# Kernel optimization log

Hardware: AMD Instinct MI355X
Metric: run time of the kernel (lower is better)

The kernel has to match this reference:

```python
import jax, jax.numpy as jnp
import numpy as np

B, L, H, SH, C = 32, 512, 1024, 50, 3   # batch, leaves, hidden, hidden_syn_size, num_classes
N = 2 * L - 1                            # total tree nodes (complete binary / heap order)
VOCAB, SYN = 30000, 128
LVLS = int(np.log2(L))                   # number of internal levels (root = level 0)


def _linear(k, fin, fout):
    lim = 1.0 / np.sqrt(fin)
    kw, kb = jax.random.split(k)
    W = jax.random.uniform(kw, (fin, fout), minval=-lim, maxval=lim, dtype=jnp.float32)
    b = jax.random.uniform(kb, (fout,), minval=-lim, maxval=lim, dtype=jnp.float32)
    return W, b


def setup_inputs() -> dict:
    key = jax.random.key(0)
    ks = jax.random.split(key, 12)
    x = jax.random.randint(ks[0], (B, N), 0, SYN)                 # node ids (word at leaves, syntax elsewhere)
    word_index = jnp.broadcast_to(jnp.arange(L - 1, 2 * L - 1), (B, L))  # leaf node indices (heap order)
    cue = jax.random.randint(ks[1], (B, N), 0, C)
    pos = jax.random.randint(ks[2], (B, L), 0, SYN)               # POS tag per leaf
    # parent->child adjacency of the heap tree, adj[:,1] is what forward reads
    A = np.zeros((N, N), dtype=bool)
    par = np.arange(L - 1)
    A[par, 2 * par + 1] = True
    A[par, 2 * par + 2] = True
    adj = jnp.broadcast_to(jnp.asarray(A)[None, None], (B, 2, N, N))
    pre_embs = jnp.zeros((1,), jnp.float32)                       # unused (use_pretrained_embs=False)
    word_emb_W = jax.random.normal(ks[3], (VOCAB, H), jnp.float32) * 0.02
    syn_emb_W = jax.random.normal(ks[4], (SYN, SH), jnp.float32) * 0.02
    leaf_W, leaf_b = _linear(ks[5], H + SH + C, H)
    comp_W, comp_b = _linear(ks[6], 2 * H + SH, H)
    grev_W, grev_b = _linear(ks[7], H + SH, H)
    dec_W, dec_b = _linear(ks[8], 2 * H + 2 * SH, 2 * H)
    clf_W, clf_b = _linear(ks[9], 2 * H, C)
    return dict(x=x, word_index=word_index, cue=cue, adj=adj, pos=pos, pre_embs=pre_embs,
                word_emb_W=word_emb_W, syn_emb_W=syn_emb_W,
                leaf_W=leaf_W, leaf_b=leaf_b, comp_W=comp_W, comp_b=comp_b,
                grev_W=grev_W, grev_b=grev_b, dec_W=dec_W, dec_b=dec_b,
                clf_W=clf_W, clf_b=clf_b)


def reference(x, word_index, cue, adj, pos, pre_embs,
              word_emb_W, syn_emb_W, leaf_W, leaf_b, comp_W, comp_b,
              grev_W, grev_b, dec_W, dec_b, clf_W, clf_b):
    # Eval-mode forward (self.training == False, so no dropout masks are applied).
    # Tree structure is the complete binary heap encoded in adj: children of i are 2i+1, 2i+2.
    b_ix = jnp.arange(B)[:, None]
    s = jnp.take_along_axis(x, word_index, axis=1)                # (B,L) leaf word ids
    c = jnp.take_along_axis(cue, word_index, axis=1)              # (B,L) leaf cue ids
    word_e = word_emb_W[s]                                        # (B,L,H)
    cue_e = jax.nn.one_hot(c, C, dtype=word_e.dtype)              # (B,L,C)
    pos_e = syn_emb_W[pos]                                        # (B,L,SH)
    x_emb = jnp.concatenate([word_e, cue_e, pos_e], -1) @ leaf_W + leaf_b  # (B,L,H), no activation

    up = jnp.zeros((B, N, H), x_emb.dtype).at[b_ix, word_index].set(x_emb)
    # upward pass: batched level-order compose (bottom internal level -> root)
    for lvl in range(LVLS - 1, -1, -1):
        nodes = jnp.arange(2 ** lvl - 1, 2 ** (lvl + 1) - 1)
        l, r = 2 * nodes + 1, 2 * nodes + 2
        cons = syn_emb_W[x[:, nodes]]                             # (B,W,SH)
        ctx = jnp.concatenate([cons, up[:, l], up[:, r]], -1)     # (B,W,SH+2H)
        up = up.at[:, nodes].set(jnp.tanh(ctx @ comp_W + comp_b))

    root_ctx = jnp.concatenate([up[:, 0], syn_emb_W[x[:, 0]]], -1)
    gd = jnp.tanh(root_ctx @ grev_W + grev_b)                     # (B,H)
    down = jnp.zeros((B, N, H), gd.dtype).at[:, 0].set(gd)
    # downward pass: batched level-order decompose (root -> leaves)
    for lvl in range(LVLS):
        nodes = jnp.arange(2 ** lvl - 1, 2 ** (lvl + 1) - 1)
        l, r = 2 * nodes + 1, 2 * nodes + 2
        if lvl == LVLS - 1:   # children are leaves -> their syntax is the POS embedding
            cons_l = pos_e[:, l - (L - 1)]
            cons_r = pos_e[:, r - (L - 1)]
        else:
            cons_l = syn_emb_W[x[:, l]]
            cons_r = syn_emb_W[x[:, r]]
        pctx = jnp.concatenate([down[:, nodes], up[:, nodes]], -1)  # (parent_emb, upward[parent])
        dctx = jnp.concatenate([cons_l, cons_r, pctx], -1)
        ch = jnp.tanh(dctx @ dec_W + dec_b)                        # (B,W,2H)
        down = down.at[:, l].set(ch[..., :H]).at[:, r].set(ch[..., H:])

    tree = jnp.concatenate([down, up], -1)                         # (B,N,2H)
    return jnp.tanh(tree @ clf_W + clf_b)                          # (B,N,C)
```

## Files before the change

### kernel.cpp

```cpp
#include <hip/hip_runtime.h>

typedef unsigned short u16;
typedef unsigned int   u32;

typedef __bf16 bf16x8 __attribute__((ext_vector_type(8)));
typedef float  f32x4  __attribute__((ext_vector_type(4)));

#define NB 1023
#define HH 1024

__device__ __forceinline__ float b2f(u16 x) { return __uint_as_float(((u32)x) << 16); }
__device__ __forceinline__ u16 f2b(float f) {
    u32 u = __float_as_uint(f);
    u += 0x7fffu + ((u >> 16) & 1u);
    return (u16)(u >> 16);
}
__device__ __forceinline__ float fast_tanh(float x) {
    float cx = fminf(fmaxf(x, -12.f), 12.f);
    float e = __expf(2.f * cx);
    return __fdividef(e - 1.f, e + 1.f);
}
__device__ __forceinline__ void async_copy16(const void* gptr, void* lptr) {
    __builtin_amdgcn_global_load_lds((__attribute__((address_space(1))) void*)gptr,
                                     (__attribute__((address_space(3))) void*)lptr,
                                     16, 0, 0);
}
__device__ __forceinline__ u16 loadAsBf16(const void* p, size_t idx, int isf32) {
    if (isf32) return f2b(((const float*)p)[idx]);
    return ((const u16*)p)[idx];
}

__device__ __forceinline__ int detect_local(const u32* __restrict__ w) {
    __shared__ int cnt;
    const int tid = threadIdx.x;
    if (tid == 0) cnt = 0;
    __syncthreads();
    u32 v = w[tid & 255];
    u32 lo = v & 0xFFFFu;
    u32 e = (lo >> 7) & 0xFFu;
    if ((lo != 0u) && (e < 60u || e > 140u)) atomicAdd(&cnt, 1);
    __syncthreads();
    return cnt >= 64;
}

__device__ void conv_range(const void* __restrict__ src, u16* __restrict__ dst,
                           int n, int tbase, int isf32) {
    const int i = ((int)blockIdx.x - tbase) * 256 + threadIdx.x;
    if (i < n) dst[i] = loadAsBf16(src, i, isf32);
}

__device__ void transpose_tile(const void* __restrict__ W, u16* __restrict__ Wt,
                               int Nw, int Kpad, int bx, int by, int isf32,
                               int ps0, int ps1, int ps2, int ps3,
                               int os0, int os1, int os2, int os3,
                               int ln0, int ln1, int ln2, int ln3)
{
    __shared__ u16 tile[32][33];
    const int tid = threadIdx.x;
    const int tx = tid & 31, ty = tid >> 5;
    #pragma unroll
    for (int i = 0; i < 4; ++i) {
        const int kp = by*32 + ty + i*8;
        const int n = bx*32 + tx;
        int ko = -1;
        if      (kp >= ps0 && kp < ps0 + ln0) ko = os0 + (kp - ps0);
        else if (kp >= ps1 && kp < ps1 + ln1) ko = os1 + (kp - ps1);
        else if (kp >= ps2 && kp < ps2 + ln2) ko = os2 + (kp - ps2);
        else if (kp >= ps3 && kp < ps3 + ln3) ko = os3 + (kp - ps3);
        u16 v = 0;
        if (ko >= 0) v = loadAsBf16(W, (size_t)ko * Nw + n, isf32);
        tile[ty + i*8][tx] = v;
    }
    __syncthreads();
    #pragma unroll
    for (int i = 0; i < 4; ++i) {
        const int n = bx*32 + ty + i*8;
        const int kp = by*32 + tx;
        Wt[(size_t)n * Kpad + kp] = tile[tx][ty + i*8];
    }
}

__global__ __launch_bounds__(256)
void preprocess(const u32* __restrict__ wembU,
                const void* __restrict__ semb,  const void* __restrict__ leafb,
                const void* __restrict__ compb, const void* __restrict__ grevb,
                const void* __restrict__ decb,  const void* __restrict__ clfb,
                const void* __restrict__ clfW,
                const void* __restrict__ leafW, const void* __restrict__ compW,
                const void* __restrict__ grevW, const void* __restrict__ decW,
                u16* __restrict__ sembP,  u16* __restrict__ leafbC,
                u16* __restrict__ compbC, u16* __restrict__ grevbC,
                u16* __restrict__ decbC,  u16* __restrict__ clfbC,
                u16* __restrict__ clfWC,
                u16* __restrict__ leafWt, u16* __restrict__ compWt,
                u16* __restrict__ grevWt, u16* __restrict__ decWt)
{
    const int isf32 = detect_local(wembU);
    const int bid = blockIdx.x;
    if (bid < 32) {
        const int i = bid * 256 + threadIdx.x;
        const int s = i >> 6, c = i & 63;
        sembP[i] = (c < 50) ? loadAsBf16(semb, s * 50 + c, isf32) : (u16)0;
    } else if (bid < 36)  conv_range(leafb, leafbC, 1024, 32, isf32);
    else if (bid < 40)  conv_range(compb, compbC, 1024, 36, isf32);
    else if (bid < 44)  conv_range(grevb, grevbC, 1024, 40, isf32);
    else if (bid < 52)  conv_range(decb,  decbC,  2048, 44, isf32);
    else if (bid < 53)  conv_range(clfb,  clfbC,  3,    52, isf32);
    else if (bid < 77)  conv_range(clfW,  clfWC,  6144, 53, isf32);
    else if (bid < 1165) {
        const int t = bid - 77;
        transpose_tile(leafW, leafWt, 1024, 1088, t & 31, t >> 5, isf32,
                       0,-1,-1,-1,  0,0,0,0,  1077,0,0,0);
    } else if (bid < 3277) {
        const int t = bid - 1165;
        transpose_tile(compW, compWt, 1024, 2112, t & 31, t >> 5, isf32,
                       0,64,1088,-1,  0,50,1074,0,  50,1024,1024,0);
    } else if (bid < 4365) {
        const int t = bid - 3277;
        transpose_tile(grevW, grevWt, 1024, 1088, t & 31, t >> 5, isf32,
                       0,1024,-1,-1,  0,1024,0,0,  1024,50,0,0);
    } else {
        const int t = bid - 4365;
        transpose_tile(decW, decWt, 2048, 2176, t & 63, t >> 6, isf32,
                       0,64,128,1152,  0,50,100,1124,  50,50,1024,1024);
    }
}

__global__ __launch_bounds__(256)
void leaf_gather(const int* __restrict__ x, const int* __restrict__ cue,
                 const int* __restrict__ pos, const void* __restrict__ wemb,
                 const u16* __restrict__ sembP, u16* __restrict__ ctx)
{
    const int isf32 = detect_local((const u32*)wemb);
    const int m = blockIdx.x;
    const int b = m >> 9, i = m & 511;
    const int node = 511 + i;
    const int s  = x[b*NB + node];
    const int cv = cue[b*NB + node];
    const int p  = pos[b*512 + i];
    u16* row = ctx + (size_t)m * 1088;
    u32* row32 = (u32*)row;
    const u16* sr = sembP + p * 64;
    const int tid = threadIdx.x;
    if (isf32) {
        const float2* wrf = ((const float2*)wemb) + (size_t)s * 512;
        for (int c = tid; c < 512; c += 256) {
            float2 t = wrf[c];
            row32[c] = (u32)f2b(t.x) | ((u32)f2b(t.y) << 16);
        }
    } else {
        const u32* wr = ((const u32*)wemb) + (size_t)s * 512;
        for (int c = tid; c < 512; c += 256) row32[c] = wr[c];
    }
    if (tid < 64) {
        const int c = tid;
        u16 v;
        if (c < 3)       v = (c == cv) ? (u16)0x3F80 : (u16)0;
        else if (c < 53) v = sr[c - 3];
        else             v = 0;
        row[1024 + c] = v;
    }
}

template<int AKIND, int MODE>
__global__ __launch_bounds__(256)
void gemm_fused(const u16* __restrict__ Bt, const u16* __restrict__ bias,
                u16* __restrict__ dst, int M, int Kpad, int nodeBase, int lognn,
                int leafLvl,
                const u16* __restrict__ actx,
                const int* __restrict__ x, const int* __restrict__ pos,
                const u16* __restrict__ sembP,
                const u16* __restrict__ upB, const u16* __restrict__ downB)
{
    __shared__ __align__(16) u16 As[2*4096];
    __shared__ __align__(16) u16 Bs[2*4096];
    const int tid  = threadIdx.x;
    const int wave = tid >> 6;
    const int lane = tid & 63;
    const int bm = blockIdx.y << 7;
    const int bn = blockIdx.x << 7;
    const int wm = (wave & 1) << 6;
    const int wn = (wave >> 1) << 6;
    const int quad = lane >> 4;
    const int l16  = lane & 15;
    const int srow = lane >> 2;
    const int scol = (lane & 3) << 3;
    const int mask = (1 << lognn) - 1;

    const u16* p0[2]; const u16* p1[2]; const u16* p2[2]; const u16* p3[2];
    #pragma unroll
    for (int h = 0; h < 2; ++h) {
        const int mrow = bm + wave*16 + srow + h*64;
        const int mr = (mrow < M) ? mrow : 0;
        if (AKIND == 0) {
            p0[h] = actx + (size_t)mr * Kpad + scol;
        } else if (AKIND == 1) {
            const int b_ = mr >> lognn, ii = mr & mask;
            const int node = nodeBase + ii;
            const int s = x[b_*NB + node];
            p0[h] = sembP + s*64 + scol;
            p1[h] = upB + (((size_t)(b_*NB + 2*node + 1)) << 10) + scol;
            p2[h] = upB + (((size_t)(b_*NB + 2*node + 2)) << 10) + scol;
        } else if (AKIND == 2) {
            p0[h] = upB + (((size_t)(mr*NB)) << 10) + scol;
            p1[h] = sembP + x[mr*NB]*64 + scol;
        } else {
            const int b_ = mr >> lognn, ii = mr & mask;
            const int node = nodeBase + ii;
            const int l = 2*node + 1, r = l + 1;
            int sli, sri;
            if (leafLvl) { sli = pos[b_*512 + (l-511)]; sri = pos[b_*512 + (r-511)]; }
            else         { sli = x[b_*NB + l]; sri = x[b_*NB + r]; }
            p0[h] = sembP + sli*64 + scol;
            p1[h] = sembP + sri*64 + scol;
            p2[h] = downB + (((size_t)(b_*NB + node)) << 10) + scol;
            p3[h] = upB   + (((size_t)(b_*NB + node)) << 10) + scol;
        }
    }

    const u16* gB0 = Bt + (size_t)(bn + wave*16 + srow) * Kpad + scol;
    const u16* gB1 = gB0 + (size_t)64 * Kpad;
    u16* lA0 = &As[wave * 512];
    u16* lA1 = &As[(wave + 4) * 512];
    u16* lB0 = &Bs[wave * 512];
    u16* lB1 = &Bs[(wave + 4) * 512];

    const u16* pa[4]; const u16* pb[4];
    #pragma unroll
    for (int i = 0; i < 4; ++i) pa[i] = &As[(wm + i*16 + l16) * 32 + quad*8];
    #pragma unroll
    for (int j = 0; j < 4; ++j) pb[j] = &Bs[(wn + j*16 + l16) * 32 + quad*8];

    f32x4 zero4 = {0.f, 0.f, 0.f, 0.f};
    f32x4 acc[4][4];
    #pragma unroll
    for (int i = 0; i < 4; ++i)
        #pragma unroll
        for (int j = 0; j < 4; ++j) acc[i][j] = zero4;

    auto kstep64 = [&](const u16* sA0, const u16* sA1, int k0) {
        async_copy16(sA0,           lA0);
        async_copy16(sA1,           lA1);
        async_copy16(gB0 + k0,      lB0);
        async_copy16(gB1 + k0,      lB1);
        async_copy16(sA0 + 32,      lA0 + 4096);
        async_copy16(sA1 + 32,      lA1 + 4096);
        async_copy16(gB0 + k0 + 32, lB0 + 4096);
        async_copy16(gB1 + k0 + 32, lB1 + 4096);
        __syncthreads();
        #pragma unroll
        for (int c = 0; c < 2; ++c) {
            bf16x8 a[4], b[4];
            #pragma unroll
            for (int i = 0; i < 4; ++i) a[i] = *(const bf16x8*)(pa[i] + c*4096);
            #pragma unroll
            for (int j = 0; j < 4; ++j) b[j] = *(const bf16x8*)(pb[j] + c*4096);
            #pragma unroll
            for (int i = 0; i < 4; ++i)
                #pragma unroll
                for (int j = 0; j < 4; ++j)
                    acc[i][j] = __builtin_amdgcn_mfma_f32_16x16x32_bf16(a[i], b[j], acc[i][j], 0, 0, 0);
        }
        __syncthreads();
    };

    if (AKIND == 0) {
        for (int k0 = 0; k0 < 1088; k0 += 64) kstep64(p0[0] + k0, p0[1] + k0, k0);
    } else if (AKIND == 1) {
        kstep64(p0[0], p0[1], 0);
        for (int k0 = 64;   k0 < 1088; k0 += 64) kstep64(p1[0] + (k0-64),   p1[1] + (k0-64),   k0);
        for (int k0 = 1088; k0 < 2112; k0 += 64) kstep64(p2[0] + (k0-1088), p2[1] + (k0-1088), k0);
    } else if (AKIND == 2) {
        for (int k0 = 0; k0 < 1024; k0 += 64) kstep64(p0[0] + k0, p0[1] + k0, k0);
        kstep64(p1[0], p1[1], 1024);
    } else {
        kstep64(p0[0], p0[1], 0);
        kstep64(p1[0], p1[1], 64);
        for (int k0 = 128;  k0 < 1152; k0 += 64) kstep64(p2[0] + (k0-128),  p2[1] + (k0-128),  k0);
        for (int k0 = 1152; k0 < 2176; k0 += 64) kstep64(p3[0] + (k0-1152), p3[1] + (k0-1152), k0);
    }

    #pragma unroll
    for (int i = 0; i < 4; ++i) {
        #pragma unroll
        for (int j = 0; j < 4; ++j) {
            const int gn = bn + wn + j*16 + l16;
            const float bv = b2f(bias[gn]);
            #pragma unroll
            for (int r = 0; r < 4; ++r) {
                const int gm = bm + wm + i*16 + quad*4 + r;
                if (gm < M) {
                    float v = acc[i][j][r] + bv;
                    if (MODE != 0) v = fast_tanh(v);
                    const int b_ = gm >> lognn;
                    const int ii = gm & mask;
                    const int node = nodeBase + ii;
                    size_t addr;
                    if (MODE == 2) {
                        const int child = 2*node + 1 + (gn >> 10);
                        addr = (((size_t)(b_*NB + child)) << 10) + (gn & 1023);
                    } else {
                        addr = (((size_t)(b_*NB + node)) << 10) + gn;
                    }
                    dst[addr] = f2b(v);
                }
            }
        }
    }
}

__global__ __launch_bounds__(256)
void classifier_kernel(const u16* __restrict__ down, const u16* __restrict__ up,
                       const u16* __restrict__ clfW, const u16* __restrict__ clfb,
                       void* __restrict__ outp, const u32* __restrict__ wembU)
{
    __shared__ float wls[3][2048];
    const int isf32 = detect_local(wembU);
    const int tid = threadIdx.x;
    for (int idx = tid; idx < 6144; idx += 256) {
        const int c = idx >> 11, k = idx & 2047;
        wls[c][k] = b2f(clfW[k*3 + c]);
    }
    __syncthreads();
    const int wave = tid >> 6, lane = tid & 63;
    const float b0 = b2f(clfb[0]), b1 = b2f(clfb[1]), b2v = b2f(clfb[2]);
    const int base = blockIdx.x * 32;
    for (int rr = 0; rr < 8; ++rr) {
        const int row = base + rr*4 + wave;
        const u32* dn = (const u32*)(down + ((size_t)row << 10));
        const u32* un = (const u32*)(up   + ((size_t)row << 10));
        float a0 = 0.f, a1 = 0.f, a2 = 0.f;
        #pragma unroll
        for (int t = 0; t < 8; ++t) {
            const int j = t*64 + lane;
            const u32 dp = dn[j], uu = un[j];
            const int k = j*2;
            const float d0 = __uint_as_float(dp << 16);
            const float d1 = __uint_as_float(dp & 0xffff0000u);
            const float u0 = __uint_as_float(uu << 16);
            const float u1 = __uint_as_float(uu & 0xffff0000u);
            a0 += d0*wls[0][k] + d1*wls[0][k+1] + u0*wls[0][1024+k] + u1*wls[0][1025+k];
            a1 += d0*wls[1][k] + d1*wls[1][k+1] + u0*wls[1][1024+k] + u1*wls[1][1025+k];
            a2 += d0*wls[2][k] + d1*wls[2][k+1] + u0*wls[2][1024+k] + u1*wls[2][1025+k];
        }
        #pragma unroll
        for (int off = 32; off; off >>= 1) {
            a0 += __shfl_down(a0, off);
            a1 += __shfl_down(a1, off);
            a2 += __shfl_down(a2, off);
        }
        if (lane == 0) {
            const float v0 = fast_tanh(a0 + b0);
            const float v1 = fast_tanh(a1 + b1);
            const float v2 = fast_tanh(a2 + b2v);
            if (isf32) {
                float* o = (float*)outp + (size_t)row * 3;
                o[0] = v0; o[1] = v1; o[2] = v2;
            } else {
                u16* o = (u16*)outp + (size_t)row * 3;
                o[0] = f2b(v0); o[1] = f2b(v1); o[2] = f2b(v2);
            }
        }
    }
}

extern "C" void kernel_launch(void* const* d_in, const int* in_sizes, int n_in,
                              void* d_out, int out_size, void* d_ws, size_t ws_size,
                              hipStream_t stream)
{
    (void)in_sizes; (void)n_in; (void)out_size; (void)ws_size;
    const int* x    = (const int*)d_in[0];
    const int* cue  = (const int*)d_in[2];
    const int* pos  = (const int*)d_in[4];
    const void* wemb  = d_in[6];
    const void* semb  = d_in[7];
    const void* leafW = d_in[8];
    const void* leafb = d_in[9];
    const void* compW = d_in[10];
    const void* compb = d_in[11];
    const void* grevW = d_in[12];
    const void* grevb = d_in[13];
    const void* decW  = d_in[14];
    const void* decb  = d_in[15];
    const void* clfW  = d_in[16];
    const void* clfb  = d_in[17];

    char* ws = (char*)d_ws;
    u16* up_buf   = (u16*)(ws + 0);
    u16* down_buf = (u16*)(ws + 67043328);
    u16* ctx      = (u16*)(ws + 134086656);
    u16* leafWt   = (u16*)(ws + 169738240);
    u16* compWt   = (u16*)(ws + 171966464);
    u16* grevWt   = (u16*)(ws + 176291840);
    u16* decWt    = (u16*)(ws + 178520064);
    u16* sembP    = (u16*)(ws + 187432960);
    u16* leafbC   = (u16*)(ws + 187449344);
    u16* compbC   = (u16*)(ws + 187451392);
    u16* grevbC   = (u16*)(ws + 187453440);
    u16* decbC    = (u16*)(ws + 187455488);
    u16* clfbC    = (u16*)(ws + 187459584);
    u16* clfWC    = (u16*)(ws + 187459600);

    preprocess<<<8717, 256, 0, stream>>>((const u32*)wemb,
        semb, leafb, compb, grevb, decb, clfb, clfW,
        leafW, compW, grevW, decW,
        sembP, leafbC, compbC, grevbC, decbC, clfbC, clfWC,
        leafWt, compWt, grevWt, decWt);

    leaf_gather<<<16384, 256, 0, stream>>>(x, cue, pos, wemb, sembP, ctx);
    gemm_fused<0,0><<<dim3(8, 128), 256, 0, stream>>>(leafWt, leafbC, up_buf,
        16384, 1088, 511, 9, 0, ctx, x, pos, sembP, up_buf, down_buf);
    for (int lvl = 8; lvl >= 0; --lvl) {
        const int M = 32 << lvl;
        const int Mpad = M < 128 ? 128 : M;
        const int first = (1 << lvl) - 1;
        gemm_fused<1,1><<<dim3(8, Mpad >> 7), 256, 0, stream>>>(compWt, compbC, up_buf,
            M, 2112, first, lvl, 0, nullptr, x, pos, sembP, up_buf, down_buf);
    }
    gemm_fused<2,1><<<dim3(8, 1), 256, 0, stream>>>(grevWt, grevbC, down_buf,
        32, 1088, 0, 0, 0, nullptr, x, pos, sembP, up_buf, down_buf);
    for (int lvl = 0; lvl <= 8; ++lvl) {
        const int M = 32 << lvl;
        const int Mpad = M < 128 ? 128 : M;
        const int first = (1 << lvl) - 1;
        gemm_fused<3,2><<<dim3(16, Mpad >> 7), 256, 0, stream>>>(decWt, decbC, down_buf,
            M, 2176, first, lvl, lvl == 8 ? 1 : 0, nullptr, x, pos, sembP, up_buf, down_buf);
    }
    classifier_kernel<<<1023, 256, 0, stream>>>(down_buf, up_buf, clfWC, clfbC,
                                                d_out, (const u32*)wemb);
}
```

Before: 1.290 ms.

## Add 128x256 wide GEMM tiles for large levels and fold leaf gather into preprocess

Adds a gemm_wide kernel with 128x256 output tiles, 64-wide K steps and a 4x8 MFMA accumulator per wave. It is used for the leaf projection, the widest compose level, and the two widest decompose levels, so each A tile is reused across more columns and there are fewer barriers per K. The leaf-context gather is merged into the preprocess launch, which removes one kernel launch. The gathered rows now read the syntax embedding directly instead of the padded copy. The larger per-thread accumulator raises register pressure, which may lower occupancy even with launch bounds of 2.

```diff
diff --git a/kernel.cpp b/kernel.cpp
--- a/kernel.cpp
+++ b/kernel.cpp
@@ -82,6 +82,8 @@
 
 __global__ __launch_bounds__(256)
 void preprocess(const u32* __restrict__ wembU,
+                const int* __restrict__ x, const int* __restrict__ cue,
+                const int* __restrict__ pos,
                 const void* __restrict__ semb,  const void* __restrict__ leafb,
                 const void* __restrict__ compb, const void* __restrict__ grevb,
                 const void* __restrict__ decb,  const void* __restrict__ clfb,
@@ -93,7 +95,8 @@
                 u16* __restrict__ decbC,  u16* __restrict__ clfbC,
                 u16* __restrict__ clfWC,
                 u16* __restrict__ leafWt, u16* __restrict__ compWt,
-                u16* __restrict__ grevWt, u16* __restrict__ decWt)
+                u16* __restrict__ grevWt, u16* __restrict__ decWt,
+                u16* __restrict__ ctx)
 {
     const int isf32 = detect_local(wembU);
     const int bid = blockIdx.x;
@@ -119,46 +122,72 @@
         const int t = bid - 3277;
         transpose_tile(grevW, grevWt, 1024, 1088, t & 31, t >> 5, isf32,
                        0,1024,-1,-1,  0,1024,0,0,  1024,50,0,0);
-    } else {
+    } else if (bid < 8717) {
         const int t = bid - 4365;
         transpose_tile(decW, decWt, 2048, 2176, t & 63, t >> 6, isf32,
                        0,64,128,1152,  0,50,100,1124,  50,50,1024,1024);
-    }
-}
-
-__global__ __launch_bounds__(256)
-void leaf_gather(const int* __restrict__ x, const int* __restrict__ cue,
-                 const int* __restrict__ pos, const void* __restrict__ wemb,
-                 const u16* __restrict__ sembP, u16* __restrict__ ctx)
-{
-    const int isf32 = detect_local((const u32*)wemb);
-    const int m = blockIdx.x;
-    const int b = m >> 9, i = m & 511;
-    const int node = 511 + i;
-    const int s  = x[b*NB + node];
-    const int cv = cue[b*NB + node];
-    const int p  = pos[b*512 + i];
-    u16* row = ctx + (size_t)m * 1088;
-    u32* row32 = (u32*)row;
-    const u16* sr = sembP + p * 64;
-    const int tid = threadIdx.x;
-    if (isf32) {
-        const float2* wrf = ((const float2*)wemb) + (size_t)s * 512;
-        for (int c = tid; c < 512; c += 256) {
-            float2 t = wrf[c];
-            row32[c] = (u32)f2b(t.x) | ((u32)f2b(t.y) << 16);
-        }
     } else {
-        const u32* wr = ((const u32*)wemb) + (size_t)s * 512;
-        for (int c = tid; c < 512; c += 256) row32[c] = wr[c];
-    }
-    if (tid < 64) {
-        const int c = tid;
-        u16 v;
-        if (c < 3)       v = (c == cv) ? (u16)0x3F80 : (u16)0;
-        else if (c < 53) v = sr[c - 3];
-        else             v = 0;
-        row[1024 + c] = v;
+        const int m = bid - 8717;
+        const int b = m >> 9, i = m & 511;
+        const int node = 511 + i;
+        const int s  = x[b*NB + node];
+        const int cv = cue[b*NB + node];
+        const int p  = pos[b*512 + i];
+        u16* row = ctx + (size_t)m * 1088;
+        u32* row32 = (u32*)row;
+        const int tid = threadIdx.x;
+        if (isf32) {
+            const float2* wrf = ((const float2*)wembU) + (size_t)s * 512;
+            for (int c = tid; c < 512; c += 256) {
+                float2 t = wrf[c];
+                row32[c] = (u32)f2b(t.x) | ((u32)f2b(t.y) << 16);
+            }
+        } else {
+            const u32* wr = ((const u32*)wembU) + (size_t)s * 512;
+            for (int c = tid; c < 512; c += 256) row32[c] = wr[c];
+        }
+        if (tid < 64) {
+            const int c = tid;
+            u16 v;
+            if (c < 3)       v = (c == cv) ? (u16)0x3F80 : (u16)0;
+            else if (c < 53) v = loadAsBf16(semb, p * 50 + (c - 3), isf32);
+            else             v = 0;
+            row[1024 + c] = v;
+        }
+    }
+}
+
+template<int AKIND>
+__device__ __forceinline__ void setup_arows(
+    int mrow, int M, int nodeBase, int lognn, int mask, int leafLvl, int scol, int Kpad,
+    const u16* __restrict__ actx, const int* __restrict__ x, const int* __restrict__ pos,
+    const u16* __restrict__ sembP, const u16* __restrict__ upB, const u16* __restrict__ downB,
+    const u16*& q0, const u16*& q1, const u16*& q2, const u16*& q3)
+{
+    const int mr = (mrow < M) ? mrow : 0;
+    if (AKIND == 0) {
+        q0 = actx + (size_t)mr * Kpad + scol;
+    } else if (AKIND == 1) {
+        const int b_ = mr >> lognn, ii = mr & mask;
+        const int node = nodeBase + ii;
+        const int s = x[b_*NB + node];
+        q0 = sembP + s*64 + scol;
+        q1 = upB + (((size_t)(b_*NB + 2*node + 1)) << 10) + scol;
+        q2 = upB + (((size_t)(b_*NB + 2*node + 2)) << 10) + scol;
+    } else if (AKIND == 2) {
+        q0 = upB + (((size_t)(mr*NB)) << 10) + scol;
+        q1 = sembP + x[mr*NB]*64 + scol;
+    } else {
+        const int b_ = mr >> lognn, ii = mr & mask;
+        const int node = nodeBase + ii;
+        const int l = 2*node + 1, r = l + 1;
+        int sli, sri;
+        if (leafLvl) { sli = pos[b_*512 + (l-511)]; sri = pos[b_*512 + (r-511)]; }
+        else         { sli = x[b_*NB + l]; sri = x[b_*NB + r]; }
+        q0 = sembP + sli*64 + scol;
+        q1 = sembP + sri*64 + scol;
+        q2 = downB + (((size_t)(b_*NB + node)) << 10) + scol;
+        q3 = upB   + (((size_t)(b_*NB + node)) << 10) + scol;
     }
 }
 
@@ -187,36 +216,12 @@
     const int scol = (lane & 3) << 3;
     const int mask = (1 << lognn) - 1;
 
-    const u16* p0[2]; const u16* p1[2]; const u16* p2[2]; const u16* p3[2];
-    #pragma unroll
-    for (int h = 0; h < 2; ++h) {
-        const int mrow = bm + wave*16 + srow + h*64;
-        const int mr = (mrow < M) ? mrow : 0;
-        if (AKIND == 0) {
-            p0[h] = actx + (size_t)mr * Kpad + scol;
-        } else if (AKIND == 1) {
-            const int b_ = mr >> lognn, ii = mr & mask;
-            const int node = nodeBase + ii;
-            const int s = x[b_*NB + node];
-            p0[h] = sembP + s*64 + scol;
-            p1[h] = upB + (((size_t)(b_*NB + 2*node + 1)) << 10) + scol;
-            p2[h] = upB + (((size_t)(b_*NB + 2*node + 2)) << 10) + scol;
-        } else if (AKIND == 2) {
-            p0[h] = upB + (((size_t)(mr*NB)) << 10) + scol;
-            p1[h] = sembP + x[mr*NB]*64 + scol;
-        } else {
-            const int b_ = mr >> lognn, ii = mr & mask;
-            const int node = nodeBase + ii;
-            const int l = 2*node + 1, r = l + 1;
-            int sli, sri;
-            if (leafLvl) { sli = pos[b_*512 + (l-511)]; sri = pos[b_*512 + (r-511)]; }
-            else         { sli = x[b_*NB + l]; sri = x[b_*NB + r]; }
-            p0[h] = sembP + sli*64 + scol;
-            p1[h] = sembP + sri*64 + scol;
-            p2[h] = downB + (((size_t)(b_*NB + node)) << 10) + scol;
-            p3[h] = upB   + (((size_t)(b_*NB + node)) << 10) + scol;
-        }
-    }
+    const u16 *p0[2], *p1[2], *p2[2], *p3[2];
+    #pragma unroll
+    for (int h = 0; h < 2; ++h)
+        setup_arows<AKIND>(bm + wave*16 + srow + h*64, M, nodeBase, lognn, mask, leafLvl,
+                           scol, Kpad, actx, x, pos, sembP, upB, downB,
+                           p0[h], p1[h], p2[h], p3[h]);
 
     const u16* gB0 = Bt + (size_t)(bn + wave*16 + srow) * Kpad + scol;
     const u16* gB1 = gB0 + (size_t)64 * Kpad;
@@ -309,6 +314,132 @@
     }
 }
 
+template<int AKIND, int MODE>
+__global__ __launch_bounds__(256, 2)
+void gemm_wide(const u16* __restrict__ Bt, const u16* __restrict__ bias,
+               u16* __restrict__ dst, int M, int Kpad, int nodeBase, int lognn,
+               int leafLvl,
+               const u16* __restrict__ actx,
+               const int* __restrict__ x, const int* __restrict__ pos,
+               const u16* __restrict__ sembP,
+               const u16* __restrict__ upB, const u16* __restrict__ downB)
+{
+    __shared__ __align__(16) u16 As[2*4096];
+    __shared__ __align__(16) u16 Bs[2*8192];
+    const int tid  = threadIdx.x;
+    const int wave = tid >> 6;
+    const int lane = tid & 63;
+    const int bm = blockIdx.y << 7;
+    const int bn = blockIdx.x << 8;
+    const int wm = (wave & 1) << 6;
+    const int wn = (wave >> 1) << 7;
+    const int quad = lane >> 4;
+    const int l16  = lane & 15;
+    const int srow = lane >> 2;
+    const int scol = (lane & 3) << 3;
+    const int mask = (1 << lognn) - 1;
+
+    const u16 *p0[2], *p1[2], *p2[2], *p3[2];
+    #pragma unroll
+    for (int h = 0; h < 2; ++h)
+        setup_arows<AKIND>(bm + wave*16 + srow + h*64, M, nodeBase, lognn, mask, leafLvl,
+                           scol, Kpad, actx, x, pos, sembP, upB, downB,
+                           p0[h], p1[h], p2[h], p3[h]);
+
+    const u16* gB[4];
+    #pragma unroll
+    for (int g = 0; g < 4; ++g)
+        gB[g] = Bt + (size_t)(bn + wave*64 + g*16 + srow) * Kpad + scol;
+    u16* lA0 = &As[wave * 512];
+    u16* lA1 = &As[(wave + 4) * 512];
+    u16* lB[4];
+    #pragma unroll
+    for (int g = 0; g < 4; ++g) lB[g] = &Bs[wave * 2048 + g * 512];
+
+    const u16* pa[4]; const u16* pb[8];
+    #pragma unroll
+    for (int i = 0; i < 4; ++i) pa[i] = &As[(wm + i*16 + l16) * 32 + quad*8];
+    #pragma unroll
+    for (int j = 0; j < 8; ++j) pb[j] = &Bs[(wn + j*16 + l16) * 32 + quad*8];
+
+    f32x4 zero4 = {0.f, 0.f, 0.f, 0.f};
+    f32x4 acc[4][8];
+    #pragma unroll
+    for (int i = 0; i < 4; ++i)
+        #pragma unroll
+        for (int j = 0; j < 8; ++j) acc[i][j] = zero4;
+
+    auto kstep64 = [&](const u16* sA0, const u16* sA1, int k0) {
+        async_copy16(sA0,      lA0);
+        async_copy16(sA1,      lA1);
+        #pragma unroll
+        for (int g = 0; g < 4; ++g) async_copy16(gB[g] + k0, lB[g]);
+        async_copy16(sA0 + 32, lA0 + 4096);
+        async_copy16(sA1 + 32, lA1 + 4096);
+        #pragma unroll
+        for (int g = 0; g < 4; ++g) async_copy16(gB[g] + k0 + 32, lB[g] + 8192);
+        __syncthreads();
+        #pragma unroll
+        for (int c = 0; c < 2; ++c) {
+            bf16x8 a[4], b[8];
+            #pragma unroll
+            for (int i = 0; i < 4; ++i) a[i] = *(const bf16x8*)(pa[i] + c*4096);
+            #pragma unroll
+            for (int j = 0; j < 8; ++j) b[j] = *(const bf16x8*)(pb[j] + c*8192);
+            #pragma unroll
+            for (int i = 0; i < 4; ++i)
+                #pragma unroll
+                for (int j = 0; j < 8; ++j)
+                    acc[i][j] = __builtin_amdgcn_mfma_f32_16x16x32_bf16(a[i], b[j], acc[i][j], 0, 0, 0);
+        }
+        __syncthreads();
+    };
+
+    if (AKIND == 0) {
+        for (int k0 = 0; k0 < 1088; k0 += 64) kstep64(p0[0] + k0, p0[1] + k0, k0);
+    } else if (AKIND == 1) {
+        kstep64(p0[0], p0[1], 0);
+        for (int k0 = 64;   k0 < 1088; k0 += 64) kstep64(p1[0] + (k0-64),   p1[1] + (k0-64),   k0);
+        for (int k0 = 1088; k0 < 2112; k0 += 64) kstep64(p2[0] + (k0-1088), p2[1] + (k0-1088), k0);
+    } else if (AKIND == 2) {
+        for (int k0 = 0; k0 < 1024; k0 += 64) kstep64(p0[0] + k0, p0[1] + k0, k0);
+        kstep64(p1[0], p1[1], 1024);
+    } else {
+        kstep64(p0[0], p0[1], 0);
+        kstep64(p1[0], p1[1], 64);
+        for (int k0 = 128;  k0 < 1152; k0 += 64) kstep64(p2[0] + (k0-128),  p2[1] + (k0-128),  k0);
+        for (int k0 = 1152; k0 < 2176; k0 += 64) kstep64(p3[0] + (k0-1152), p3[1] + (k0-1152), k0);
+    }
+
+    #pragma unroll
+    for (int i = 0; i < 4; ++i) {
+        #pragma unroll
+        for (int j = 0; j < 8; ++j) {
+            const int gn = bn + wn + j*16 + l16;
+            const float bv = b2f(bias[gn]);
+            #pragma unroll
+            for (int r = 0; r < 4; ++r) {
+                const int gm = bm + wm + i*16 + quad*4 + r;
+                if (gm < M) {
+                    float v = acc[i][j][r] + bv;
+                    if (MODE != 0) v = fast_tanh(v);
+                    const int b_ = gm >> lognn;
+                    const int ii = gm & mask;
+                    const int node = nodeBase + ii;
+                    size_t addr;
+                    if (MODE == 2) {
+                        const int child = 2*node + 1 + (gn >> 10);
+                        addr = (((size_t)(b_*NB + child)) << 10) + (gn & 1023);
+                    } else {
+                        addr = (((size_t)(b_*NB + node)) << 10) + gn;
+                    }
+                    dst[addr] = f2b(v);
+                }
+            }
+        }
+    }
+}
+
 __global__ __launch_bounds__(256)
 void classifier_kernel(const u16* __restrict__ down, const u16* __restrict__ up,
                        const u16* __restrict__ clfW, const u16* __restrict__ clfb,
@@ -401,16 +532,17 @@
     u16* clfbC    = (u16*)(ws + 187459584);
     u16* clfWC    = (u16*)(ws + 187459600);
 
-    preprocess<<<8717, 256, 0, stream>>>((const u32*)wemb,
+    preprocess<<<25101, 256, 0, stream>>>((const u32*)wemb, x, cue, pos,
         semb, leafb, compb, grevb, decb, clfb, clfW,
         leafW, compW, grevW, decW,
         sembP, leafbC, compbC, grevbC, decbC, clfbC, clfWC,
-        leafWt, compWt, grevWt, decWt);
-
-    leaf_gather<<<16384, 256, 0, stream>>>(x, cue, pos, wemb, sembP, ctx);
-    gemm_fused<0,0><<<dim3(8, 128), 256, 0, stream>>>(leafWt, leafbC, up_buf,
+        leafWt, compWt, grevWt, decWt, ctx);
+
+    gemm_wide<0,0><<<dim3(4, 128), 256, 0, stream>>>(leafWt, leafbC, up_buf,
         16384, 1088, 511, 9, 0, ctx, x, pos, sembP, up_buf, down_buf);
-    for (int lvl = 8; lvl >= 0; --lvl) {
+    gemm_wide<1,1><<<dim3(4, 64), 256, 0, stream>>>(compWt, compbC, up_buf,
+        8192, 2112, 255, 8, 0, nullptr, x, pos, sembP, up_buf, down_buf);
+    for (int lvl = 7; lvl >= 0; --lvl) {
         const int M = 32 << lvl;
         const int Mpad = M < 128 ? 128 : M;
         const int first = (1 << lvl) - 1;
@@ -419,13 +551,17 @@
     }
     gemm_fused<2,1><<<dim3(8, 1), 256, 0, stream>>>(grevWt, grevbC, down_buf,
         32, 1088, 0, 0, 0, nullptr, x, pos, sembP, up_buf, down_buf);
-    for (int lvl = 0; lvl <= 8; ++lvl) {
+    for (int lvl = 0; lvl <= 6; ++lvl) {
         const int M = 32 << lvl;
         const int Mpad = M < 128 ? 128 : M;
         const int first = (1 << lvl) - 1;
         gemm_fused<3,2><<<dim3(16, Mpad >> 7), 256, 0, stream>>>(decWt, decbC, down_buf,
-            M, 2176, first, lvl, lvl == 8 ? 1 : 0, nullptr, x, pos, sembP, up_buf, down_buf);
-    }
+            M, 2176, first, lvl, 0, nullptr, x, pos, sembP, up_buf, down_buf);
+    }
+    gemm_wide<3,2><<<dim3(8, 32), 256, 0, stream>>>(decWt, decbC, down_buf,
+        4096, 2176, 127, 7, 0, nullptr, x, pos, sembP, up_buf, down_buf);
+    gemm_wide<3,2><<<dim3(8, 64), 256, 0, stream>>>(decWt, decbC, down_buf,
+        8192, 2176, 255, 8, 1, nullptr, x, pos, sembP, up_buf, down_buf);
     classifier_kernel<<<1023, 256, 0, stream>>>(down_buf, up_buf, clfWC, clfbC,
                                                 d_out, (const u32*)wemb);
 }
```

Result: slower. 1.343 ms (+4.1%).
